# Kernel tuning notes

Measured on AMD Instinct MI355X. Metric: run time of the kernel, lower is better.

Reference implementation:

```python
import jax, jax.numpy as jnp
import numpy as np

N = 20000          # graph_size
IN_DIM = 256
H, D = 3, 64       # num_heads (hardcoded 3 in source), out_dim
E = 640000         # N * avg_degree(32)
NEG_SLOPE = 0.2    # DGL GATConv default negative_slope


def setup_inputs() -> dict:
    key = jax.random.key(0)
    ks = jax.random.split(key, 8)
    feat = jax.random.normal(ks[0], (N, IN_DIM), dtype=jnp.float32)
    W = jax.random.normal(ks[1], (IN_DIM, H * D), dtype=jnp.float32) * 0.05
    attn_l = jax.random.normal(ks[2], (H, D), dtype=jnp.float32) * 0.05
    attn_r = jax.random.normal(ks[3], (H, D), dtype=jnp.float32) * 0.05
    gat_bias = jnp.zeros((H * D,), dtype=jnp.float32)
    fc_w = jax.random.normal(ks[4], (N * H * D, 2), dtype=jnp.float32) * 0.001
    fc_b = jnp.zeros((2,), dtype=jnp.float32)
    src = jax.random.randint(ks[5], (E,), 0, N, dtype=jnp.int64)
    dst = jax.random.randint(ks[6], (E,), 0, N, dtype=jnp.int64)
    return {"feat": feat, "W": W, "attn_l": attn_l, "attn_r": attn_r,
            "gat_bias": gat_bias, "fc_w": fc_w, "fc_b": fc_b,
            "src": src, "dst": dst}


def reference(feat, W, attn_l, attn_r, gat_bias, fc_w, fc_b, src, dst):
    n = feat.shape[0]
    # GATConv: projected multi-head features [N, H, D]
    h = (feat @ W).reshape(n, H, D)
    el = jnp.einsum('nhd,hd->nh', h, attn_l)   # [N, H]
    er = jnp.einsum('nhd,hd->nh', h, attn_r)   # [N, H]
    # per-edge raw attention logits, LeakyReLU(el[src] + er[dst])
    e = jax.nn.leaky_relu(el[src] + er[dst], negative_slope=NEG_SLOPE)  # [E, H]
    # edge-softmax grouped by destination node (stable)
    m = jax.ops.segment_max(e, dst, num_segments=n)   # [N, H]
    ex = jnp.exp(e - m[dst])
    denom = jax.ops.segment_sum(ex, dst, num_segments=n)  # [N, H]
    alpha = ex / denom[dst]                            # [E, H]
    # weighted message aggregation: out[v] = sum_{(u->v)} alpha * h[u]
    msg = h[src] * alpha[:, :, None]                   # [E, H, D]
    out = jax.ops.segment_sum(msg, dst, num_segments=n)  # [N, H, D]
    out = out + gat_bias.reshape(H, D)                 # GATConv bias
    out = jax.nn.relu(out)                             # self.activation
    # Flatten(start_dim=0) -> Linear(N*H*D, 2)
    return out.reshape(-1) @ fc_w + fc_b               # [2]
```

## Files before the change

### kernel.cpp

```cpp
#include <hip/hip_runtime.h>
#include <hip/hip_bf16.h>
#include <cstdint>
#include <cstddef>

#define INDIM  256
#define HD     192
#define NHEADS 3
#define NEG_SLOPE 0.2f
#define ELLPAD 96
#define BSHIFT 7
#define NBUCK  160
#define BCAP   4608
#define P1CHUNK 2048

typedef __attribute__((ext_vector_type(8))) short short8;
typedef __attribute__((ext_vector_type(4))) float f32x4;

__device__ __forceinline__ float wave_sum(float v) {
#pragma unroll
    for (int o = 32; o; o >>= 1) v += __shfl_xor(v, o, 64);
    return v;
}

__global__ __launch_bounds__(256) void prep_kernel(
    const float* __restrict__ W, __hip_bfloat16* __restrict__ Wt,
    int* __restrict__ gCur)
{
    const int b = blockIdx.x, tid = threadIdx.x;
    if (b == 0) {
        if (tid < NBUCK) gCur[tid] = 0;
        return;
    }
    int n = b - 1;
    Wt[n * 256 + tid] = __float2bfloat16(W[tid * HD + n]);
}

__global__ __launch_bounds__(256) void gemm_bucket_kernel(
    const float* __restrict__ feat,
    const __hip_bfloat16* __restrict__ Wt,
    const float* __restrict__ attn_l, const float* __restrict__ attn_r,
    __hip_bfloat16* __restrict__ hb, float* __restrict__ el,
    float* __restrict__ er, int M,
    const int* __restrict__ src, const int* __restrict__ dst,
    int* __restrict__ gCur, int2* __restrict__ pairs,
    int E, int gemmBlocks)
{
    const int tid = threadIdx.x;
    if (blockIdx.x >= gemmBlocks) {
        __shared__ int cnt[NBUCK];
        __shared__ int base[NBUCK];
        const int e0 = (blockIdx.x - gemmBlocks) * P1CHUNK;
        if (tid < NBUCK) cnt[tid] = 0;
        __syncthreads();
        int d[8], s[8], b[8], l[8];
#pragma unroll
        for (int u = 0; u < 8; u++) {
            int e = e0 + u * 256 + tid;
            if (e < E) {
                d[u] = dst[e]; s[u] = src[e];
                b[u] = d[u] >> BSHIFT;
                l[u] = atomicAdd(&cnt[b[u]], 1);
            } else b[u] = -1;
        }
        __syncthreads();
        if (tid < NBUCK && cnt[tid] > 0) base[tid] = atomicAdd(&gCur[tid], cnt[tid]);
        __syncthreads();
#pragma unroll
        for (int u = 0; u < 8; u++) {
            if (b[u] >= 0) {
                int idx = base[b[u]] + l[u];
                if (idx < BCAP)
                    pairs[(size_t)b[u] * BCAP + idx] = make_int2(d[u], s[u]);
            }
        }
        return;
    }
    __shared__ __hip_bfloat16 As[64][40];
    __shared__ __hip_bfloat16 Bs[192][40];
    const int lane = tid & 63, w = tid >> 6;
    const int q = lane >> 4, ll = lane & 15;
    const int row0 = blockIdx.x * 64;

    f32x4 acc[12];
#pragma unroll
    for (int c = 0; c < 12; c++) acc[c] = (f32x4){0.f, 0.f, 0.f, 0.f};

    const int sr = tid >> 2, sk = (tid & 3) * 8;

    for (int k0 = 0; k0 < INDIM; k0 += 32) {
        __syncthreads();
        float4 a0 = make_float4(0.f, 0.f, 0.f, 0.f), a1 = a0;
        int grow = row0 + sr;
        if (grow < M) {
            const float* ap = feat + (size_t)grow * INDIM + k0 + sk;
            a0 = *(const float4*)ap;
            a1 = *(const float4*)(ap + 4);
        }
        __hip_bfloat16 ab[8] = {__float2bfloat16(a0.x), __float2bfloat16(a0.y),
                                __float2bfloat16(a0.z), __float2bfloat16(a0.w),
                                __float2bfloat16(a1.x), __float2bfloat16(a1.y),
                                __float2bfloat16(a1.z), __float2bfloat16(a1.w)};
        *(uint4*)&As[sr][sk] = *(const uint4*)ab;
        if (tid < HD) {
            const __hip_bfloat16* bp = Wt + (size_t)tid * INDIM + k0;
            uint4 b0 = *(const uint4*)bp;
            uint4 b1 = *(const uint4*)(bp + 8);
            uint4 b2 = *(const uint4*)(bp + 16);
            uint4 b3 = *(const uint4*)(bp + 24);
            *(uint4*)&Bs[tid][0]  = b0;
            *(uint4*)&Bs[tid][8]  = b1;
            *(uint4*)&Bs[tid][16] = b2;
            *(uint4*)&Bs[tid][24] = b3;
        }
        __syncthreads();

        short8 af = *(const short8*)&As[w * 16 + ll][q * 8];
#pragma unroll
        for (int c = 0; c < 12; c++) {
            short8 bf = *(const short8*)&Bs[c * 16 + ll][q * 8];
            acc[c] = __builtin_amdgcn_mfma_f32_16x16x32_bf16(af, bf, acc[c], 0, 0, 0);
        }
    }

    float al[12], ar[12];
#pragma unroll
    for (int c = 0; c < 12; c++) {
        al[c] = attn_l[c * 16 + ll];
        ar[c] = attn_r[c * 16 + ll];
    }
    float sl[3][4], sr_[3][4];
#pragma unroll
    for (int hd = 0; hd < 3; hd++)
#pragma unroll
        for (int i = 0; i < 4; i++) {
            float a = 0.f, b = 0.f;
#pragma unroll
            for (int f = 0; f < 4; f++) {
                a = fmaf(acc[hd * 4 + f][i], al[hd * 4 + f], a);
                b = fmaf(acc[hd * 4 + f][i], ar[hd * 4 + f], b);
            }
            sl[hd][i] = a; sr_[hd][i] = b;
        }
#pragma unroll
    for (int hd = 0; hd < 3; hd++)
#pragma unroll
        for (int i = 0; i < 4; i++)
#pragma unroll
            for (int off = 1; off < 16; off <<= 1) {
                sl[hd][i]  += __shfl_xor(sl[hd][i],  off, 64);
                sr_[hd][i] += __shfl_xor(sr_[hd][i], off, 64);
            }
#pragma unroll
    for (int c = 0; c < 12; c++)
#pragma unroll
        for (int i = 0; i < 4; i++) {
            int row = row0 + w * 16 + q * 4 + i;
            if (row < M)
                hb[(size_t)row * HD + c * 16 + ll] = __float2bfloat16(acc[c][i]);
        }
    if (ll == 0) {
#pragma unroll
        for (int i = 0; i < 4; i++) {
            int row = row0 + w * 16 + q * 4 + i;
            if (row < M) {
#pragma unroll
                for (int hd = 0; hd < 3; hd++) {
                    el[row * 3 + hd] = sl[hd][i];
                    er[row * 3 + hd] = sr_[hd][i];
                }
            }
        }
    }
}

__global__ __launch_bounds__(256) void ell_build_kernel(
    const int2* __restrict__ pairs, const int* __restrict__ gCur,
    int* __restrict__ ell, int* __restrict__ deg, int N)
{
    __shared__ int cur[128];
    const int b = blockIdx.x;
    const int tid = threadIdx.x;
    if (tid < 128) cur[tid] = 0;
    __syncthreads();
    const int cnt = min(gCur[b], BCAP);
    const int2* pp = pairs + (size_t)b * BCAP;
    for (int i = tid; i < cnt; i += 256) {
        int2 p = pp[i];
        int r = atomicAdd(&cur[p.x & 127], 1);
        if (r < ELLPAD) ell[(size_t)p.x * ELLPAD + r] = p.y;
    }
    __syncthreads();
    int node = (b << BSHIFT) + tid;
    if (tid < 128 && node < N) deg[node] = min(cur[tid], ELLPAD);
}

__global__ __launch_bounds__(256) void gat_node_kernel(
    const __hip_bfloat16* __restrict__ h, const float* __restrict__ el,
    const float* __restrict__ er, const int* __restrict__ deg,
    const int* __restrict__ ell, const float* __restrict__ gbias,
    const float* __restrict__ fc_w, float* __restrict__ pA,
    float* __restrict__ pB, int N)
{
    __shared__ float4 sE[4][64];

    const int tid = threadIdx.x;
    const int lane = tid & 63, wslot = tid >> 6;
    const int v = blockIdx.x * 4 + wslot;
    if (v >= N) return;

    const int cnt = deg[v];
    const int* rowp = ell + (size_t)v * ELLPAD;
    const float er0 = er[v * 3 + 0], er1 = er[v * 3 + 1], er2 = er[v * 3 + 2];

    float acc0 = 0.f, acc1 = 0.f, acc2 = 0.f;
    float d0 = 0.f, d1 = 0.f, d2 = 0.f;
    const __hip_bfloat16* hl = h + lane;

    for (int chunk = 0; chunk < cnt; chunk += 64) {
        const int i = chunk + lane;
        float w0 = 0.f, w1 = 0.f, w2 = 0.f;
        int s = 0;
        if (i < cnt) {
            s = rowp[i];
            const float* ep = el + s * 3;
            float l0 = ep[0] + er0;
            float l1 = ep[1] + er1;
            float l2 = ep[2] + er2;
            l0 = l0 > 0.f ? l0 : NEG_SLOPE * l0;
            l1 = l1 > 0.f ? l1 : NEG_SLOPE * l1;
            l2 = l2 > 0.f ? l2 : NEG_SLOPE * l2;
            w0 = __expf(l0); w1 = __expf(l1); w2 = __expf(l2);
        }
        d0 += w0; d1 += w1; d2 += w2;
        sE[wslot][lane] = make_float4(__int_as_float(s), w0, w1, w2);
        __asm__ volatile("s_waitcnt lgkmcnt(0)" ::: "memory");

        const int rem = min(cnt - chunk, 64);
        const int nR = (rem + 7) & ~7;
        for (int j = 0; j < nR; j += 8) {
            float4 e[8];
#pragma unroll
            for (int u = 0; u < 8; u++) e[u] = sE[wslot][j + u];
            float x0[8], x1[8], x2[8];
#pragma unroll
            for (int u = 0; u < 8; u++) {
                const __hip_bfloat16* p = hl + (size_t)__float_as_int(e[u].x) * HD;
                x0[u] = __bfloat162float(p[0]);
                x1[u] = __bfloat162float(p[64]);
                x2[u] = __bfloat162float(p[128]);
            }
#pragma unroll
            for (int u = 0; u < 8; u++) {
                acc0 = fmaf(e[u].y, x0[u], acc0);
                acc1 = fmaf(e[u].z, x1[u], acc1);
                acc2 = fmaf(e[u].w, x2[u], acc2);
            }
        }
    }

    d0 = wave_sum(d0); d1 = wave_sum(d1); d2 = wave_sum(d2);

    float o0 = (d0 > 0.f) ? acc0 / d0 : 0.f;
    float o1 = (d1 > 0.f) ? acc1 / d1 : 0.f;
    float o2 = (d2 > 0.f) ? acc2 / d2 : 0.f;
    o0 = fmaxf(o0 + gbias[lane], 0.f);
    o1 = fmaxf(o1 + gbias[64 + lane], 0.f);
    o2 = fmaxf(o2 + gbias[128 + lane], 0.f);

    const size_t bidx = (size_t)v * HD;
    float2 w0v = ((const float2*)fc_w)[bidx + lane];
    float2 w1v = ((const float2*)fc_w)[bidx + 64 + lane];
    float2 w2v = ((const float2*)fc_w)[bidx + 128 + lane];
    float f0 = fmaf(o0, w0v.x, fmaf(o1, w1v.x, o2 * w2v.x));
    float f1 = fmaf(o0, w0v.y, fmaf(o1, w1v.y, o2 * w2v.y));

    f0 = wave_sum(f0); f1 = wave_sum(f1);
    if (lane == 0) { pA[v] = f0; pB[v] = f1; }
}

__global__ __launch_bounds__(1024) void final_reduce(const float* __restrict__ pA,
                                                     const float* __restrict__ pB,
                                                     const float* __restrict__ fc_b,
                                                     float* __restrict__ out, int nb)
{
    int tid = threadIdx.x;
    float s0 = 0.f, s1 = 0.f;
    for (int i = tid; i < nb; i += 1024) { s0 += pA[i]; s1 += pB[i]; }
    s0 = wave_sum(s0); s1 = wave_sum(s1);
    __shared__ float sh[32];
    int lane = tid & 63, w = tid >> 6;
    if (lane == 0) { sh[w * 2] = s0; sh[w * 2 + 1] = s1; }
    __syncthreads();
    if (tid == 0) {
        float t0 = 0.f, t1 = 0.f;
#pragma unroll
        for (int i = 0; i < 16; i++) { t0 += sh[i * 2]; t1 += sh[i * 2 + 1]; }
        out[0] = t0 + fc_b[0];
        out[1] = t1 + fc_b[1];
    }
}

extern "C" void kernel_launch(void* const* d_in, const int* in_sizes, int n_in,
                              void* d_out, int out_size, void* d_ws, size_t ws_size,
                              hipStream_t stream)
{
    const float* feat   = (const float*)d_in[0];
    const float* W      = (const float*)d_in[1];
    const float* attn_l = (const float*)d_in[2];
    const float* attn_r = (const float*)d_in[3];
    const float* gbias  = (const float*)d_in[4];
    const float* fc_w   = (const float*)d_in[5];
    const float* fc_b   = (const float*)d_in[6];
    const int*   src    = (const int*)d_in[7];
    const int*   dst    = (const int*)d_in[8];

    const int N = in_sizes[0] / INDIM;
    const int E = in_sizes[7];
    const int nBuck = (N + 127) >> BSHIFT;

    __hip_bfloat16* Wt = (__hip_bfloat16*)d_ws;
    __hip_bfloat16* hb = Wt + HD * INDIM;
    float* el = (float*)(hb + (size_t)N * HD);
    float* er = el + (size_t)N * 3;
    int* gCur = (int*)(er + (size_t)N * 3);
    int* deg  = gCur + NBUCK;
    int* ell  = deg + N;
    int2* pairs = (int2*)(ell + (size_t)N * ELLPAD);
    float* pA = (float*)(pairs + (size_t)NBUCK * BCAP);
    float* pB = pA + N;

    prep_kernel<<<1 + HD, 256, 0, stream>>>(W, Wt, gCur);

    const int gemmBlocks = (N + 63) / 64;
    const int p1Blocks = (E + P1CHUNK - 1) / P1CHUNK;
    gemm_bucket_kernel<<<gemmBlocks + p1Blocks, 256, 0, stream>>>(
        feat, Wt, attn_l, attn_r, hb, el, er, N,
        src, dst, gCur, pairs, E, gemmBlocks);

    ell_build_kernel<<<nBuck, 256, 0, stream>>>(pairs, gCur, ell, deg, N);

    gat_node_kernel<<<(N + 3) / 4, 256, 0, stream>>>(hb, el, er, deg, ell,
                                                     gbias, fc_w, pA, pB, N);
    final_reduce<<<1, 1024, 0, stream>>>(pA, pB, fc_b, (float*)d_out, N);
}
```

Measured before the change: 164.9 us.

## Replace atomic bucket scatter with per-chunk prefix sums and vectorize gather

Edge bucketing no longer uses global atomics into fixed-capacity buckets. Each chunk computes a block-level prefix scan of bucket counts, writes its pairs contiguously and records per-chunk offsets, and the ELL build walks every chunk's slice for its bucket. Separately, el is padded to float4 and the aggregation loop has 48 lanes each load 4 bf16 values as one uint2, with vectorized bias and fc_w reads. This removes global atomic contention and overflow risk, but the ELL build now loops serially over ~313 chunks per thread, which may be slow and leaves ELL order nondeterministic.

Result: slower. 171.4 us (+3.9%).

```diff
diff --git a/kernel.cpp b/kernel.cpp
--- a/kernel.cpp
+++ b/kernel.cpp
@@ -10,7 +10,6 @@
 #define ELLPAD 96
 #define BSHIFT 7
 #define NBUCK  160
-#define BCAP   4608
 #define P1CHUNK 2048
 
 typedef __attribute__((ext_vector_type(8))) short short8;
@@ -23,34 +22,30 @@
 }
 
 __global__ __launch_bounds__(256) void prep_kernel(
-    const float* __restrict__ W, __hip_bfloat16* __restrict__ Wt,
-    int* __restrict__ gCur)
-{
-    const int b = blockIdx.x, tid = threadIdx.x;
-    if (b == 0) {
-        if (tid < NBUCK) gCur[tid] = 0;
-        return;
-    }
-    int n = b - 1;
-    Wt[n * 256 + tid] = __float2bfloat16(W[tid * HD + n]);
+    const float* __restrict__ W, __hip_bfloat16* __restrict__ Wt)
+{
+    const int n = blockIdx.x;
+    const int k = threadIdx.x;
+    Wt[n * 256 + k] = __float2bfloat16(W[k * HD + n]);
 }
 
 __global__ __launch_bounds__(256) void gemm_bucket_kernel(
     const float* __restrict__ feat,
     const __hip_bfloat16* __restrict__ Wt,
     const float* __restrict__ attn_l, const float* __restrict__ attn_r,
-    __hip_bfloat16* __restrict__ hb, float* __restrict__ el,
+    __hip_bfloat16* __restrict__ hb, float* __restrict__ el4,
     float* __restrict__ er, int M,
     const int* __restrict__ src, const int* __restrict__ dst,
-    int* __restrict__ gCur, int2* __restrict__ pairs,
+    int2* __restrict__ pairs, int* __restrict__ chunkPref,
     int E, int gemmBlocks)
 {
     const int tid = threadIdx.x;
     if (blockIdx.x >= gemmBlocks) {
-        __shared__ int cnt[NBUCK];
-        __shared__ int base[NBUCK];
-        const int e0 = (blockIdx.x - gemmBlocks) * P1CHUNK;
-        if (tid < NBUCK) cnt[tid] = 0;
+        __shared__ int cnt[256];
+        __shared__ int pref[256];
+        const int c = blockIdx.x - gemmBlocks;
+        const int e0 = c * P1CHUNK;
+        cnt[tid] = 0;
         __syncthreads();
         int d[8], s[8], b[8], l[8];
 #pragma unroll
@@ -63,15 +58,23 @@
             } else b[u] = -1;
         }
         __syncthreads();
-        if (tid < NBUCK && cnt[tid] > 0) base[tid] = atomicAdd(&gCur[tid], cnt[tid]);
-        __syncthreads();
+        const int val = cnt[tid];
+        for (int off = 1; off < 256; off <<= 1) {
+            int other = (tid >= off) ? cnt[tid - off] : 0;
+            __syncthreads();
+            cnt[tid] += other;
+            __syncthreads();
+        }
+        const int excl = cnt[tid] - val;
+        if (tid < NBUCK) chunkPref[c * (NBUCK + 1) + tid] = excl;
+        if (tid == 255) chunkPref[c * (NBUCK + 1) + NBUCK] = cnt[255];
+        pref[tid] = excl;
+        __syncthreads();
+        int2* pp = pairs + (size_t)c * P1CHUNK;
 #pragma unroll
         for (int u = 0; u < 8; u++) {
-            if (b[u] >= 0) {
-                int idx = base[b[u]] + l[u];
-                if (idx < BCAP)
-                    pairs[(size_t)b[u] * BCAP + idx] = make_int2(d[u], s[u]);
-            }
+            if (b[u] >= 0)
+                pp[pref[b[u]] + l[u]] = make_int2(d[u], s[u]);
         }
         return;
     }
@@ -163,31 +166,34 @@
         for (int i = 0; i < 4; i++) {
             int row = row0 + w * 16 + q * 4 + i;
             if (row < M) {
-#pragma unroll
-                for (int hd = 0; hd < 3; hd++) {
-                    el[row * 3 + hd] = sl[hd][i];
-                    er[row * 3 + hd] = sr_[hd][i];
-                }
+                *(float4*)&el4[row * 4] =
+                    make_float4(sl[0][i], sl[1][i], sl[2][i], 0.f);
+                er[row * 3 + 0] = sr_[0][i];
+                er[row * 3 + 1] = sr_[1][i];
+                er[row * 3 + 2] = sr_[2][i];
             }
         }
     }
 }
 
 __global__ __launch_bounds__(256) void ell_build_kernel(
-    const int2* __restrict__ pairs, const int* __restrict__ gCur,
-    int* __restrict__ ell, int* __restrict__ deg, int N)
+    const int2* __restrict__ pairs, const int* __restrict__ chunkPref,
+    int* __restrict__ ell, int* __restrict__ deg, int N, int nChunks)
 {
     __shared__ int cur[128];
     const int b = blockIdx.x;
     const int tid = threadIdx.x;
     if (tid < 128) cur[tid] = 0;
     __syncthreads();
-    const int cnt = min(gCur[b], BCAP);
-    const int2* pp = pairs + (size_t)b * BCAP;
-    for (int i = tid; i < cnt; i += 256) {
-        int2 p = pp[i];
-        int r = atomicAdd(&cur[p.x & 127], 1);
-        if (r < ELLPAD) ell[(size_t)p.x * ELLPAD + r] = p.y;
+    for (int c = tid; c < nChunks; c += 256) {
+        const int* cp = chunkPref + c * (NBUCK + 1) + b;
+        int st = cp[0], en = cp[1];
+        const int2* pp = pairs + (size_t)c * P1CHUNK;
+        for (int i = st; i < en; i++) {
+            int2 p = pp[i];
+            int r = atomicAdd(&cur[p.x & 127], 1);
+            if (r < ELLPAD) ell[(size_t)p.x * ELLPAD + r] = p.y;
+        }
     }
     __syncthreads();
     int node = (b << BSHIFT) + tid;
@@ -195,7 +201,7 @@
 }
 
 __global__ __launch_bounds__(256) void gat_node_kernel(
-    const __hip_bfloat16* __restrict__ h, const float* __restrict__ el,
+    const __hip_bfloat16* __restrict__ h, const float* __restrict__ el4,
     const float* __restrict__ er, const int* __restrict__ deg,
     const int* __restrict__ ell, const float* __restrict__ gbias,
     const float* __restrict__ fc_w, float* __restrict__ pA,
@@ -212,9 +218,11 @@
     const int* rowp = ell + (size_t)v * ELLPAD;
     const float er0 = er[v * 3 + 0], er1 = er[v * 3 + 1], er2 = er[v * 3 + 2];
 
-    float acc0 = 0.f, acc1 = 0.f, acc2 = 0.f;
+    const bool act = lane < 48;
+    const int hsel = lane >> 4;
+
+    float a0 = 0.f, a1 = 0.f, a2 = 0.f, a3 = 0.f;
     float d0 = 0.f, d1 = 0.f, d2 = 0.f;
-    const __hip_bfloat16* hl = h + lane;
 
     for (int chunk = 0; chunk < cnt; chunk += 64) {
         const int i = chunk + lane;
@@ -222,10 +230,10 @@
         int s = 0;
         if (i < cnt) {
             s = rowp[i];
-            const float* ep = el + s * 3;
-            float l0 = ep[0] + er0;
-            float l1 = ep[1] + er1;
-            float l2 = ep[2] + er2;
+            float4 e4 = ((const float4*)el4)[s];
+            float l0 = e4.x + er0;
+            float l1 = e4.y + er1;
+            float l2 = e4.z + er2;
             l0 = l0 > 0.f ? l0 : NEG_SLOPE * l0;
             l1 = l1 > 0.f ? l1 : NEG_SLOPE * l1;
             l2 = l2 > 0.f ? l2 : NEG_SLOPE * l2;
@@ -241,38 +249,47 @@
             float4 e[8];
 #pragma unroll
             for (int u = 0; u < 8; u++) e[u] = sE[wslot][j + u];
-            float x0[8], x1[8], x2[8];
-#pragma unroll
-            for (int u = 0; u < 8; u++) {
-                const __hip_bfloat16* p = hl + (size_t)__float_as_int(e[u].x) * HD;
-                x0[u] = __bfloat162float(p[0]);
-                x1[u] = __bfloat162float(p[64]);
-                x2[u] = __bfloat162float(p[128]);
+            if (act) {
+                uint2 x[8];
+#pragma unroll
+                for (int u = 0; u < 8; u++) {
+                    const uint2* p =
+                        (const uint2*)(h + (size_t)__float_as_int(e[u].x) * HD);
+                    x[u] = p[lane];
+                }
+#pragma unroll
+                for (int u = 0; u < 8; u++) {
+                    float wv = (hsel == 0) ? e[u].y : ((hsel == 1) ? e[u].z : e[u].w);
+                    float f0 = __uint_as_float(x[u].x << 16);
+                    float f1 = __uint_as_float(x[u].x & 0xffff0000u);
+                    float f2 = __uint_as_float(x[u].y << 16);
+                    float f3 = __uint_as_float(x[u].y & 0xffff0000u);
+                    a0 = fmaf(wv, f0, a0);
+                    a1 = fmaf(wv, f1, a1);
+                    a2 = fmaf(wv, f2, a2);
+                    a3 = fmaf(wv, f3, a3);
+                }
             }
-#pragma unroll
-            for (int u = 0; u < 8; u++) {
-                acc0 = fmaf(e[u].y, x0[u], acc0);
-                acc1 = fmaf(e[u].z, x1[u], acc1);
-                acc2 = fmaf(e[u].w, x2[u], acc2);
-            }
         }
     }
 
     d0 = wave_sum(d0); d1 = wave_sum(d1); d2 = wave_sum(d2);
 
-    float o0 = (d0 > 0.f) ? acc0 / d0 : 0.f;
-    float o1 = (d1 > 0.f) ? acc1 / d1 : 0.f;
-    float o2 = (d2 > 0.f) ? acc2 / d2 : 0.f;
-    o0 = fmaxf(o0 + gbias[lane], 0.f);
-    o1 = fmaxf(o1 + gbias[64 + lane], 0.f);
-    o2 = fmaxf(o2 + gbias[128 + lane], 0.f);
-
-    const size_t bidx = (size_t)v * HD;
-    float2 w0v = ((const float2*)fc_w)[bidx + lane];
-    float2 w1v = ((const float2*)fc_w)[bidx + 64 + lane];
-    float2 w2v = ((const float2*)fc_w)[bidx + 128 + lane];
-    float f0 = fmaf(o0, w0v.x, fmaf(o1, w1v.x, o2 * w2v.x));
-    float f1 = fmaf(o0, w0v.y, fmaf(o1, w1v.y, o2 * w2v.y));
+    float f0 = 0.f, f1 = 0.f;
+    if (act) {
+        float dd = (hsel == 0) ? d0 : ((hsel == 1) ? d1 : d2);
+        float inv = (dd > 0.f) ? 1.f / dd : 0.f;
+        float4 gb = ((const float4*)gbias)[lane];
+        float o0 = fmaxf(a0 * inv + gb.x, 0.f);
+        float o1 = fmaxf(a1 * inv + gb.y, 0.f);
+        float o2 = fmaxf(a2 * inv + gb.z, 0.f);
+        float o3 = fmaxf(a3 * inv + gb.w, 0.f);
+        const float4* fw = (const float4*)(fc_w + ((size_t)v * HD + 4 * lane) * 2);
+        float4 wa = fw[0];
+        float4 wb = fw[1];
+        f0 = fmaf(o0, wa.x, fmaf(o1, wa.z, fmaf(o2, wb.x, o3 * wb.z)));
+        f1 = fmaf(o0, wa.y, fmaf(o1, wa.w, fmaf(o2, wb.y, o3 * wb.w)));
+    }
 
     f0 = wave_sum(f0); f1 = wave_sum(f1);
     if (lane == 0) { pA[v] = f0; pB[v] = f1; }
@@ -316,30 +333,30 @@
 
     const int N = in_sizes[0] / INDIM;
     const int E = in_sizes[7];
-    const int nBuck = (N + 127) >> BSHIFT;
+    const int nBuck  = (N + 127) >> BSHIFT;
+    const int p1Blocks = (E + P1CHUNK - 1) / P1CHUNK;
 
     __hip_bfloat16* Wt = (__hip_bfloat16*)d_ws;
     __hip_bfloat16* hb = Wt + HD * INDIM;
-    float* el = (float*)(hb + (size_t)N * HD);
-    float* er = el + (size_t)N * 3;
-    int* gCur = (int*)(er + (size_t)N * 3);
-    int* deg  = gCur + NBUCK;
-    int* ell  = deg + N;
-    int2* pairs = (int2*)(ell + (size_t)N * ELLPAD);
-    float* pA = (float*)(pairs + (size_t)NBUCK * BCAP);
+    float* el4 = (float*)(hb + (size_t)N * HD);
+    float* er  = el4 + (size_t)N * 4;
+    int*   deg = (int*)(er + (size_t)N * 3);
+    int*   ell = deg + N;
+    int2*  pairs = (int2*)(ell + (size_t)N * ELLPAD);
+    int*   chunkPref = (int*)(pairs + (size_t)p1Blocks * P1CHUNK);
+    float* pA = (float*)(chunkPref + (size_t)p1Blocks * (NBUCK + 1) + 3);
     float* pB = pA + N;
 
-    prep_kernel<<<1 + HD, 256, 0, stream>>>(W, Wt, gCur);
+    prep_kernel<<<HD, 256, 0, stream>>>(W, Wt);
 
     const int gemmBlocks = (N + 63) / 64;
-    const int p1Blocks = (E + P1CHUNK - 1) / P1CHUNK;
     gemm_bucket_kernel<<<gemmBlocks + p1Blocks, 256, 0, stream>>>(
-        feat, Wt, attn_l, attn_r, hb, el, er, N,
-        src, dst, gCur, pairs, E, gemmBlocks);
-
-    ell_build_kernel<<<nBuck, 256, 0, stream>>>(pairs, gCur, ell, deg, N);
-
-    gat_node_kernel<<<(N + 3) / 4, 256, 0, stream>>>(hb, el, er, deg, ell,
+        feat, Wt, attn_l, attn_r, hb, el4, er, N,
+        src, dst, pairs, chunkPref, E, gemmBlocks);
+
+    ell_build_kernel<<<nBuck, 256, 0, stream>>>(pairs, chunkPref, ell, deg, N, p1Blocks);
+
+    gat_node_kernel<<<(N + 3) / 4, 256, 0, stream>>>(hb, el4, er, deg, ell,
                                                      gbias, fc_w, pA, pB, N);
     final_reduce<<<1, 1024, 0, stream>>>(pA, pB, fc_b, (float*)d_out, N);
 }
```

## Pack edge pairs, pad el/er to float4, fuse final reduction via last-block

Applied to the files above, without the earlier changes.

Edge bucket entries are packed into a single int (local dst in the high bits, src in the low 15 bits), which halves the pairs traffic. el/er are padded to float4 so each gather is one vector load. The separate final_reduce launch is removed: each gat block writes a partial sum, and the last block, found through an atomic counter, does the final sum. The bucketing chunk is also halved to spread atomics over more blocks. Packing assumes N < 32768, and the counter adds an atomic plus fences per block.

Result: slower. 317.0 us (+92.2%).

```diff
diff --git a/kernel.cpp b/kernel.cpp
--- a/kernel.cpp
+++ b/kernel.cpp
@@ -11,7 +11,7 @@
 #define BSHIFT 7
 #define NBUCK  160
 #define BCAP   4608
-#define P1CHUNK 2048
+#define P1CHUNK 1024
 
 typedef __attribute__((ext_vector_type(8))) short short8;
 typedef __attribute__((ext_vector_type(4))) float f32x4;
@@ -28,7 +28,7 @@
 {
     const int b = blockIdx.x, tid = threadIdx.x;
     if (b == 0) {
-        if (tid < NBUCK) gCur[tid] = 0;
+        if (tid <= NBUCK) gCur[tid] = 0;
         return;
     }
     int n = b - 1;
@@ -39,10 +39,10 @@
     const float* __restrict__ feat,
     const __hip_bfloat16* __restrict__ Wt,
     const float* __restrict__ attn_l, const float* __restrict__ attn_r,
-    __hip_bfloat16* __restrict__ hb, float* __restrict__ el,
-    float* __restrict__ er, int M,
+    __hip_bfloat16* __restrict__ hb, float* __restrict__ el4,
+    float* __restrict__ er4, int M,
     const int* __restrict__ src, const int* __restrict__ dst,
-    int* __restrict__ gCur, int2* __restrict__ pairs,
+    int* __restrict__ gCur, int* __restrict__ pairs,
     int E, int gemmBlocks)
 {
     const int tid = threadIdx.x;
@@ -52,13 +52,14 @@
         const int e0 = (blockIdx.x - gemmBlocks) * P1CHUNK;
         if (tid < NBUCK) cnt[tid] = 0;
         __syncthreads();
-        int d[8], s[8], b[8], l[8];
-#pragma unroll
-        for (int u = 0; u < 8; u++) {
+        int pk[4], b[4], l[4];
+#pragma unroll
+        for (int u = 0; u < 4; u++) {
             int e = e0 + u * 256 + tid;
             if (e < E) {
-                d[u] = dst[e]; s[u] = src[e];
-                b[u] = d[u] >> BSHIFT;
+                int d = dst[e];
+                b[u] = d >> BSHIFT;
+                pk[u] = ((d & 127) << 15) | src[e];
                 l[u] = atomicAdd(&cnt[b[u]], 1);
             } else b[u] = -1;
         }
@@ -66,11 +67,11 @@
         if (tid < NBUCK && cnt[tid] > 0) base[tid] = atomicAdd(&gCur[tid], cnt[tid]);
         __syncthreads();
 #pragma unroll
-        for (int u = 0; u < 8; u++) {
+        for (int u = 0; u < 4; u++) {
             if (b[u] >= 0) {
                 int idx = base[b[u]] + l[u];
                 if (idx < BCAP)
-                    pairs[(size_t)b[u] * BCAP + idx] = make_int2(d[u], s[u]);
+                    pairs[(size_t)b[u] * BCAP + idx] = pk[u];
             }
         }
         return;
@@ -163,18 +164,17 @@
         for (int i = 0; i < 4; i++) {
             int row = row0 + w * 16 + q * 4 + i;
             if (row < M) {
-#pragma unroll
-                for (int hd = 0; hd < 3; hd++) {
-                    el[row * 3 + hd] = sl[hd][i];
-                    er[row * 3 + hd] = sr_[hd][i];
-                }
+                *(float4*)&el4[row * 4] =
+                    make_float4(sl[0][i], sl[1][i], sl[2][i], 0.f);
+                *(float4*)&er4[row * 4] =
+                    make_float4(sr_[0][i], sr_[1][i], sr_[2][i], 0.f);
             }
         }
     }
 }
 
 __global__ __launch_bounds__(256) void ell_build_kernel(
-    const int2* __restrict__ pairs, const int* __restrict__ gCur,
+    const int* __restrict__ pairs, const int* __restrict__ gCur,
     int* __restrict__ ell, int* __restrict__ deg, int N)
 {
     __shared__ int cur[128];
@@ -183,120 +183,131 @@
     if (tid < 128) cur[tid] = 0;
     __syncthreads();
     const int cnt = min(gCur[b], BCAP);
-    const int2* pp = pairs + (size_t)b * BCAP;
+    const int* pp = pairs + (size_t)b * BCAP;
+    const int node0 = b << BSHIFT;
     for (int i = tid; i < cnt; i += 256) {
-        int2 p = pp[i];
-        int r = atomicAdd(&cur[p.x & 127], 1);
-        if (r < ELLPAD) ell[(size_t)p.x * ELLPAD + r] = p.y;
+        int p = pp[i];
+        int dl = p >> 15;
+        int r = atomicAdd(&cur[dl], 1);
+        if (r < ELLPAD) ell[(size_t)(node0 + dl) * ELLPAD + r] = p & 0x7FFF;
     }
     __syncthreads();
-    int node = (b << BSHIFT) + tid;
+    int node = node0 + tid;
     if (tid < 128 && node < N) deg[node] = min(cur[tid], ELLPAD);
 }
 
 __global__ __launch_bounds__(256) void gat_node_kernel(
-    const __hip_bfloat16* __restrict__ h, const float* __restrict__ el,
-    const float* __restrict__ er, const int* __restrict__ deg,
+    const __hip_bfloat16* __restrict__ h, const float* __restrict__ el4,
+    const float* __restrict__ er4, const int* __restrict__ deg,
     const int* __restrict__ ell, const float* __restrict__ gbias,
-    const float* __restrict__ fc_w, float* __restrict__ pA,
-    float* __restrict__ pB, int N)
+    const float* __restrict__ fc_w, const float* __restrict__ fc_b,
+    float* __restrict__ pBlk, int* __restrict__ doneCnt,
+    float* __restrict__ out, int N)
 {
     __shared__ float4 sE[4][64];
+    __shared__ float sf[8];
+    __shared__ int   lastFlag;
 
     const int tid = threadIdx.x;
     const int lane = tid & 63, wslot = tid >> 6;
     const int v = blockIdx.x * 4 + wslot;
-    if (v >= N) return;
-
-    const int cnt = deg[v];
-    const int* rowp = ell + (size_t)v * ELLPAD;
-    const float er0 = er[v * 3 + 0], er1 = er[v * 3 + 1], er2 = er[v * 3 + 2];
-
-    float acc0 = 0.f, acc1 = 0.f, acc2 = 0.f;
-    float d0 = 0.f, d1 = 0.f, d2 = 0.f;
-    const __hip_bfloat16* hl = h + lane;
-
-    for (int chunk = 0; chunk < cnt; chunk += 64) {
-        const int i = chunk + lane;
-        float w0 = 0.f, w1 = 0.f, w2 = 0.f;
-        int s = 0;
-        if (i < cnt) {
-            s = rowp[i];
-            const float* ep = el + s * 3;
-            float l0 = ep[0] + er0;
-            float l1 = ep[1] + er1;
-            float l2 = ep[2] + er2;
-            l0 = l0 > 0.f ? l0 : NEG_SLOPE * l0;
-            l1 = l1 > 0.f ? l1 : NEG_SLOPE * l1;
-            l2 = l2 > 0.f ? l2 : NEG_SLOPE * l2;
-            w0 = __expf(l0); w1 = __expf(l1); w2 = __expf(l2);
-        }
-        d0 += w0; d1 += w1; d2 += w2;
-        sE[wslot][lane] = make_float4(__int_as_float(s), w0, w1, w2);
-        __asm__ volatile("s_waitcnt lgkmcnt(0)" ::: "memory");
-
-        const int rem = min(cnt - chunk, 64);
-        const int nR = (rem + 7) & ~7;
-        for (int j = 0; j < nR; j += 8) {
-            float4 e[8];
-#pragma unroll
-            for (int u = 0; u < 8; u++) e[u] = sE[wslot][j + u];
-            float x0[8], x1[8], x2[8];
-#pragma unroll
-            for (int u = 0; u < 8; u++) {
-                const __hip_bfloat16* p = hl + (size_t)__float_as_int(e[u].x) * HD;
-                x0[u] = __bfloat162float(p[0]);
-                x1[u] = __bfloat162float(p[64]);
-                x2[u] = __bfloat162float(p[128]);
-            }
-#pragma unroll
-            for (int u = 0; u < 8; u++) {
-                acc0 = fmaf(e[u].y, x0[u], acc0);
-                acc1 = fmaf(e[u].z, x1[u], acc1);
-                acc2 = fmaf(e[u].w, x2[u], acc2);
-            }
-        }
-    }
-
-    d0 = wave_sum(d0); d1 = wave_sum(d1); d2 = wave_sum(d2);
-
-    float o0 = (d0 > 0.f) ? acc0 / d0 : 0.f;
-    float o1 = (d1 > 0.f) ? acc1 / d1 : 0.f;
-    float o2 = (d2 > 0.f) ? acc2 / d2 : 0.f;
-    o0 = fmaxf(o0 + gbias[lane], 0.f);
-    o1 = fmaxf(o1 + gbias[64 + lane], 0.f);
-    o2 = fmaxf(o2 + gbias[128 + lane], 0.f);
-
-    const size_t bidx = (size_t)v * HD;
-    float2 w0v = ((const float2*)fc_w)[bidx + lane];
-    float2 w1v = ((const float2*)fc_w)[bidx + 64 + lane];
-    float2 w2v = ((const float2*)fc_w)[bidx + 128 + lane];
-    float f0 = fmaf(o0, w0v.x, fmaf(o1, w1v.x, o2 * w2v.x));
-    float f1 = fmaf(o0, w0v.y, fmaf(o1, w1v.y, o2 * w2v.y));
+
+    float f0 = 0.f, f1 = 0.f;
+    if (v < N) {
+        const int cnt = deg[v];
+        const int* rowp = ell + (size_t)v * ELLPAD;
+        float4 erv = ((const float4*)er4)[v];
+        const float er0 = erv.x, er1 = erv.y, er2 = erv.z;
+
+        float acc0 = 0.f, acc1 = 0.f, acc2 = 0.f;
+        float d0 = 0.f, d1 = 0.f, d2 = 0.f;
+        const __hip_bfloat16* hl = h + lane;
+
+        for (int chunk = 0; chunk < cnt; chunk += 64) {
+            const int i = chunk + lane;
+            float w0 = 0.f, w1 = 0.f, w2 = 0.f;
+            int s = 0;
+            if (i < cnt) {
+                s = rowp[i];
+                float4 e4 = ((const float4*)el4)[s];
+                float l0 = e4.x + er0;
+                float l1 = e4.y + er1;
+                float l2 = e4.z + er2;
+                l0 = l0 > 0.f ? l0 : NEG_SLOPE * l0;
+                l1 = l1 > 0.f ? l1 : NEG_SLOPE * l1;
+                l2 = l2 > 0.f ? l2 : NEG_SLOPE * l2;
+                w0 = __expf(l0); w1 = __expf(l1); w2 = __expf(l2);
+            }
+            d0 += w0; d1 += w1; d2 += w2;
+            sE[wslot][lane] = make_float4(__int_as_float(s), w0, w1, w2);
+            __asm__ volatile("s_waitcnt lgkmcnt(0)" ::: "memory");
+
+            const int rem = min(cnt - chunk, 64);
+            const int nR = (rem + 7) & ~7;
+            for (int j = 0; j < nR; j += 8) {
+                float4 e[8];
+#pragma unroll
+                for (int u = 0; u < 8; u++) e[u] = sE[wslot][j + u];
+                float x0[8], x1[8], x2[8];
+#pragma unroll
+                for (int u = 0; u < 8; u++) {
+                    const __hip_bfloat16* p = hl + (size_t)__float_as_int(e[u].x) * HD;
+                    x0[u] = __bfloat162float(p[0]);
+                    x1[u] = __bfloat162float(p[64]);
+                    x2[u] = __bfloat162float(p[128]);
+                }
+#pragma unroll
+                for (int u = 0; u < 8; u++) {
+                    acc0 = fmaf(e[u].y, x0[u], acc0);
+                    acc1 = fmaf(e[u].z, x1[u], acc1);
+                    acc2 = fmaf(e[u].w, x2[u], acc2);
+                }
+            }
+        }
+
+        d0 = wave_sum(d0); d1 = wave_sum(d1); d2 = wave_sum(d2);
+
+        float o0 = (d0 > 0.f) ? acc0 / d0 : 0.f;
+        float o1 = (d1 > 0.f) ? acc1 / d1 : 0.f;
+        float o2 = (d2 > 0.f) ? acc2 / d2 : 0.f;
+        o0 = fmaxf(o0 + gbias[lane], 0.f);
+        o1 = fmaxf(o1 + gbias[64 + lane], 0.f);
+        o2 = fmaxf(o2 + gbias[128 + lane], 0.f);
+
+        const size_t bidx = (size_t)v * HD;
+        float2 w0v = ((const float2*)fc_w)[bidx + lane];
+        float2 w1v = ((const float2*)fc_w)[bidx + 64 + lane];
+        float2 w2v = ((const float2*)fc_w)[bidx + 128 + lane];
+        f0 = fmaf(o0, w0v.x, fmaf(o1, w1v.x, o2 * w2v.x));
+        f1 = fmaf(o0, w0v.y, fmaf(o1, w1v.y, o2 * w2v.y));
+    }
 
     f0 = wave_sum(f0); f1 = wave_sum(f1);
-    if (lane == 0) { pA[v] = f0; pB[v] = f1; }
-}
-
-__global__ __launch_bounds__(1024) void final_reduce(const float* __restrict__ pA,
-                                                     const float* __restrict__ pB,
-                                                     const float* __restrict__ fc_b,
-                                                     float* __restrict__ out, int nb)
-{
-    int tid = threadIdx.x;
-    float s0 = 0.f, s1 = 0.f;
-    for (int i = tid; i < nb; i += 1024) { s0 += pA[i]; s1 += pB[i]; }
-    s0 = wave_sum(s0); s1 = wave_sum(s1);
-    __shared__ float sh[32];
-    int lane = tid & 63, w = tid >> 6;
-    if (lane == 0) { sh[w * 2] = s0; sh[w * 2 + 1] = s1; }
+    if (lane == 0) { sf[wslot * 2] = f0; sf[wslot * 2 + 1] = f1; }
     __syncthreads();
     if (tid == 0) {
-        float t0 = 0.f, t1 = 0.f;
-#pragma unroll
-        for (int i = 0; i < 16; i++) { t0 += sh[i * 2]; t1 += sh[i * 2 + 1]; }
-        out[0] = t0 + fc_b[0];
-        out[1] = t1 + fc_b[1];
+        pBlk[blockIdx.x * 2 + 0] = sf[0] + sf[2] + sf[4] + sf[6];
+        pBlk[blockIdx.x * 2 + 1] = sf[1] + sf[3] + sf[5] + sf[7];
+        __threadfence();
+        int old = atomicAdd(doneCnt, 1);
+        lastFlag = (old == (int)gridDim.x - 1);
+    }
+    __syncthreads();
+    if (lastFlag) {
+        __threadfence();
+        float s0 = 0.f, s1 = 0.f;
+        const int nb = gridDim.x;
+        for (int i = tid; i < nb; i += 256) {
+            s0 += pBlk[i * 2 + 0];
+            s1 += pBlk[i * 2 + 1];
+        }
+        s0 = wave_sum(s0); s1 = wave_sum(s1);
+        if (lane == 0) { sf[wslot * 2] = s0; sf[wslot * 2 + 1] = s1; }
+        __syncthreads();
+        if (tid == 0) {
+            out[0] = sf[0] + sf[2] + sf[4] + sf[6] + fc_b[0];
+            out[1] = sf[1] + sf[3] + sf[5] + sf[7] + fc_b[1];
+        }
     }
 }
 
@@ -320,26 +331,26 @@
 
     __hip_bfloat16* Wt = (__hip_bfloat16*)d_ws;
     __hip_bfloat16* hb = Wt + HD * INDIM;
-    float* el = (float*)(hb + (size_t)N * HD);
-    float* er = el + (size_t)N * 3;
-    int* gCur = (int*)(er + (size_t)N * 3);
-    int* deg  = gCur + NBUCK;
+    float* el4 = (float*)(hb + (size_t)N * HD);
+    float* er4 = el4 + (size_t)N * 4;
+    int* gCur = (int*)(er4 + (size_t)N * 4);
+    int* deg  = gCur + NBUCK + 4;
     int* ell  = deg + N;
-    int2* pairs = (int2*)(ell + (size_t)N * ELLPAD);
-    float* pA = (float*)(pairs + (size_t)NBUCK * BCAP);
-    float* pB = pA + N;
+    int* pairs = ell + (size_t)N * ELLPAD;
+    float* pBlk = (float*)(pairs + (size_t)NBUCK * BCAP);
 
     prep_kernel<<<1 + HD, 256, 0, stream>>>(W, Wt, gCur);
 
     const int gemmBlocks = (N + 63) / 64;
     const int p1Blocks = (E + P1CHUNK - 1) / P1CHUNK;
     gemm_bucket_kernel<<<gemmBlocks + p1Blocks, 256, 0, stream>>>(
-        feat, Wt, attn_l, attn_r, hb, el, er, N,
+        feat, Wt, attn_l, attn_r, hb, el4, er4, N,
         src, dst, gCur, pairs, E, gemmBlocks);
 
     ell_build_kernel<<<nBuck, 256, 0, stream>>>(pairs, gCur, ell, deg, N);
 
-    gat_node_kernel<<<(N + 3) / 4, 256, 0, stream>>>(hb, el, er, deg, ell,
-                                                     gbias, fc_w, pA, pB, N);
-    final_reduce<<<1, 1024, 0, stream>>>(pA, pB, fc_b, (float*)d_out, N);
-}
+    const int gatBlocks = (N + 3) / 4;
+    gat_node_kernel<<<gatBlocks, 256, 0, stream>>>(hb, el4, er4, deg, ell,
+                                                   gbias, fc_w, fc_b,
+                                                   pBlk, gCur + NBUCK, (float*)d_out, N);
+}
```
